# Optimization experiments

Hardware: AMD Instinct MI355X
Metric: run time of the kernel (lower is better)

## Reference

```python
import jax, jax.numpy as jnp
import numpy as np

N = 100000        # nodes
E = 3200000       # edges (avg in-degree ~32)
NG = 64           # graphs in batch
F_IN = 64         # num_node_features
AVG_LOG = float(np.log(33.0))   # avg log-degree baked from deg (avg degree 32)
BN_EPS = 1e-5
STD_EPS = 1e-5

def _glorot(key, fi, fo):
    lim = float(np.sqrt(6.0 / (fi + fo)))
    return jax.random.uniform(key, (fi, fo), jnp.float32, -lim, lim)

def setup_inputs():
    key = jax.random.key(0)
    ks = jax.random.split(key, 16)
    inp = {
        'x': jax.random.normal(ks[0], (N, F_IN), jnp.float32),
        'edge_index': jax.random.randint(ks[1], (2, E), 0, N),
        'batch': jnp.sort(jax.random.randint(ks[2], (N,), 0, NG)),
    }
    dims = [(F_IN, 96), (96, 64), (64, 32), (32, 20)]
    for i, (fi, fo) in enumerate(dims):
        inp[f'w{i}'] = _glorot(ks[3 + i], 13 * fi, fo)  # (4 aggr * 3 scalers + 1 self) * F_in
        inp[f'b{i}'] = jnp.zeros((fo,), jnp.float32)
    for i, c in enumerate([96, 64, 20]):
        inp[f'g{i}'] = jnp.ones((c,), jnp.float32)
        inp[f'be{i}'] = jnp.zeros((c,), jnp.float32)
    inp['w_lin'] = _glorot(ks[10], 20, 11)
    inp['b_lin'] = jnp.zeros((11,), jnp.float32)
    return inp

def _pna_layer(x, src, dst, cnt, degc, W, b):
    m = x[src]                                          # [E, F] gather of neighbor feats
    inv = (1.0 / degc)[:, None]
    mean = jax.ops.segment_sum(m, dst, N) * inv
    mean_sq = jax.ops.segment_sum(m * m, dst, N) * inv
    std = jnp.sqrt(jax.nn.relu(mean_sq - mean * mean) + STD_EPS)
    has = (cnt > 0)[:, None]
    mn = jnp.where(has, jax.ops.segment_min(m, dst, N), 0.0)
    mx = jnp.where(has, jax.ops.segment_max(m, dst, N), 0.0)
    agg = jnp.concatenate([mean, mn, mx, std], axis=-1)  # [N, 4F]
    logd = jnp.log(degc + 1.0)[:, None]
    out = jnp.concatenate([agg, agg * (logd / AVG_LOG), agg * (AVG_LOG / logd)], axis=-1)  # [N, 12F]
    out = jnp.concatenate([x, out], axis=-1)             # [N, 13F] self + scaled aggregations
    return out @ W + b

def _bn(x, g, b):
    mu = x.mean(0)
    var = x.var(0)  # biased var: matches torch BatchNorm training forward
    return (x - mu) * jax.lax.rsqrt(var + BN_EPS) * g + b

def _forward(x, edge_index, batch, w0, b0, w1, b1, w2, b2, w3, b3,
             g0, be0, g1, be1, g2, be2, w_lin, b_lin):
    src, dst = edge_index[0], edge_index[1]
    cnt = jax.ops.segment_sum(jnp.ones((E,), x.dtype), dst, N)  # in-degree
    degc = jnp.maximum(cnt, 1.0)
    h = jax.nn.relu(_bn(_pna_layer(x, src, dst, cnt, degc, w0, b0), g0, be0))
    h = jax.nn.relu(_bn(_pna_layer(h, src, dst, cnt, degc, w1, b1), g1, be1))
    h = jax.nn.relu(_pna_layer(h, src, dst, cnt, degc, w2, b2))
    h = _bn(_pna_layer(h, src, dst, cnt, degc, w3, b3), g2, be2)
    gcnt = jnp.maximum(jax.ops.segment_sum(jnp.ones((N,), h.dtype), batch, NG), 1.0)
    z = jax.ops.segment_sum(h, batch, NG) / gcnt[:, None]       # global mean pool [NG, 20]
    out = jax.nn.softmax(z @ w_lin + b_lin, axis=-1)            # dropout identity (eval)
    return out, z

def reference(x, edge_index, batch, w0, b0, w1, b1, w2, b2, w3, b3,
              g0, be0, g1, be1, g2, be2, w_lin, b_lin):
    return _forward(x, edge_index, batch, w0, b0, w1, b1, w2, b2, w3, b3,
                    g0, be0, g1, be1, g2, be2, w_lin, b_lin)
```

## Files before the change

kernel.cpp:

```cpp
#include <hip/hip_runtime.h>

#define NN 100000
#define NGRAPH 64
#define NPART 8
#define NPB 12500
#define DB 16
#define PW_C 2048
#define AVGLOG 3.4965075614664802f

using f32x2 = __attribute__((ext_vector_type(2))) float;
using f32x4 = __attribute__((ext_vector_type(4))) float;
using f16x2 = __attribute__((ext_vector_type(2))) _Float16;
using f16x8 = __attribute__((ext_vector_type(8))) _Float16;
using f16x4 = __attribute__((ext_vector_type(4))) _Float16;
using i32x4 = __attribute__((ext_vector_type(4))) int;

__global__ __launch_bounds__(256) void k_pcnt(const int* __restrict__ ei,
                                              int* __restrict__ pcnt, int E, int W) {
  const int w = blockIdx.x * 4 + (threadIdx.x >> 6);
  const int lane = threadIdx.x & 63;
  if (w >= W) return;
  int c[NPART];
#pragma unroll
  for (int b = 0; b < NPART; ++b) c[b] = 0;
  const long long base = (long long)w * PW_C;
  for (int r = 0; r < PW_C / 256; ++r) {
    long long e0 = base + r * 256 + lane * 4;
    int bk[4] = {-1, -1, -1, -1};
    if (e0 + 3 < E) {
      i32x4 d = __builtin_nontemporal_load((const i32x4*)(ei + E + e0));
#pragma unroll
      for (int k = 0; k < 4; ++k) bk[k] = d[k] / NPB;
    } else {
#pragma unroll
      for (int k = 0; k < 4; ++k)
        if (e0 + k < E) bk[k] = ei[E + e0 + k] / NPB;
    }
#pragma unroll
    for (int b = 0; b < NPART; ++b) {
      int t = 0;
#pragma unroll
      for (int k = 0; k < 4; ++k) t += __popcll(__ballot(bk[k] == b));
      c[b] += t;
    }
  }
  if (lane == 0) {
#pragma unroll
    for (int b = 0; b < NPART; ++b) pcnt[w * NPART + b] = c[b];
  }
}

__global__ void k_pscan(const int* __restrict__ pcnt, int* __restrict__ pbase,
                        int* __restrict__ bcur, int W) {
  __shared__ int s[256];
  __shared__ int btot[NPART];
  const int t = threadIdx.x;
  const int per = (W + 255) / 256;
  for (int b = 0; b < NPART; ++b) {
    int loc = 0;
    const int w0 = t * per;
    for (int i = 0; i < per; ++i) {
      int w = w0 + i;
      if (w < W) loc += pcnt[w * NPART + b];
    }
    s[t] = loc;
    __syncthreads();
    for (int off = 1; off < 256; off <<= 1) {
      int u = (t >= off) ? s[t - off] : 0;
      __syncthreads();
      s[t] += u;
      __syncthreads();
    }
    int run = s[t] - loc;
    if (t == 255) btot[b] = s[255];
    for (int i = 0; i < per; ++i) {
      int w = w0 + i;
      if (w < W) {
        pbase[w * NPART + b] = run;
        run += pcnt[w * NPART + b];
      }
    }
    __syncthreads();
  }
  if (t < NPART) bcur[t] = btot[t];
}

__global__ __launch_bounds__(256) void k_pbin(const int* __restrict__ ei,
                                              const int* __restrict__ pbase,
                                              unsigned long long* __restrict__ bkt,
                                              int cap, int E, int W) {
  const int w = blockIdx.x * 4 + (threadIdx.x >> 6);
  const int lane = threadIdx.x & 63;
  if (w >= W) return;
  int off[NPART];
#pragma unroll
  for (int b = 0; b < NPART; ++b) off[b] = pbase[w * NPART + b];
  const unsigned long long lmask = (1ull << lane) - 1ull;
  const long long base = (long long)w * PW_C;
  for (int r = 0; r < PW_C / 256; ++r) {
    long long e0 = base + r * 256 + lane * 4;
    int bk[4] = {-1, -1, -1, -1};
    int sv[4], dv[4];
    if (e0 + 3 < E) {
      i32x4 d = __builtin_nontemporal_load((const i32x4*)(ei + E + e0));
      i32x4 s4 = __builtin_nontemporal_load((const i32x4*)(ei + e0));
#pragma unroll
      for (int k = 0; k < 4; ++k) { dv[k] = d[k]; sv[k] = s4[k]; bk[k] = d[k] / NPB; }
    } else {
#pragma unroll
      for (int k = 0; k < 4; ++k)
        if (e0 + k < E) { dv[k] = ei[E + e0 + k]; sv[k] = ei[e0 + k]; bk[k] = dv[k] / NPB; }
    }
#pragma unroll
    for (int k = 0; k < 4; ++k) {
#pragma unroll
      for (int b = 0; b < NPART; ++b) {
        unsigned long long m = __ballot(bk[k] == b);
        if (bk[k] == b) {
          int idx = off[b] + __popcll(m & lmask);
          bkt[(size_t)b * cap + idx] =
              ((unsigned long long)(unsigned)dv[k] << 32) | (unsigned)sv[k];
        }
        off[b] += __popcll(m);
      }
    }
  }
}

__global__ __launch_bounds__(256) void k_dhist(
    const unsigned long long* __restrict__ bkt, const int* __restrict__ bcur,
    int cap, int* __restrict__ dhist) {
  __shared__ int hist[NPB];
  const int p = blockIdx.x & (NPART - 1);
  const int b = blockIdx.x >> 3;
  const int tid = threadIdx.x;
  for (int i = tid; i < NPB; i += 256) hist[i] = 0;
  __syncthreads();
  const int n = bcur[p];
  const int chunk = (n + DB - 1) / DB;
  const int lo = b * chunk, hi = min(n, lo + chunk);
  const unsigned long long* base = bkt + (size_t)p * cap;
  const int plo = p * NPB;
  for (int i = lo + tid; i < hi; i += 256) {
    unsigned long long v = base[i];
    atomicAdd(&hist[(int)(v >> 32) - plo], 1);
  }
  __syncthreads();
  int* dst = dhist + ((size_t)p * DB + b) * NPB;
  for (int i = tid; i < NPB; i += 256) dst[i] = hist[i];
}

__global__ void k_mergesum(int* __restrict__ dhist, int* __restrict__ cnt,
                           int* __restrict__ bsum, int n) {
  __shared__ int s[256];
  int i = blockIdx.x * 256 + threadIdx.x;
  int acc = 0;
  if (i < n) {
    int p = i / NPB, li = i - p * NPB;
    int* hb = dhist + (size_t)p * DB * NPB + li;
#pragma unroll
    for (int b = 0; b < DB; ++b) {
      int t = hb[b * NPB];
      hb[b * NPB] = acc;
      acc += t;
    }
    cnt[i] = acc;
  }
  s[threadIdx.x] = acc;
  __syncthreads();
  for (int off = 128; off > 0; off >>= 1) {
    if (threadIdx.x < off) s[threadIdx.x] += s[threadIdx.x + off];
    __syncthreads();
  }
  if (threadIdx.x == 0) bsum[blockIdx.x] = s[0];
}

__global__ __launch_bounds__(256) void k_binfill(
    const unsigned long long* __restrict__ bkt, const int* __restrict__ bcur,
    int cap, const int* __restrict__ dhist, const int* __restrict__ row_ptr,
    int* __restrict__ colv) {
  __shared__ int rank[NPB];
  const int p = blockIdx.x & (NPART - 1);
  const int b = blockIdx.x >> 3;
  const int tid = threadIdx.x;
  const int plo = p * NPB;
  const int* soff = dhist + ((size_t)p * DB + b) * NPB;
  for (int li = tid; li < NPB; li += 256) rank[li] = row_ptr[plo + li] + soff[li];
  __syncthreads();
  const int n = bcur[p];
  const int chunk = (n + DB - 1) / DB;
  const int lo = b * chunk, hi = min(n, lo + chunk);
  const unsigned long long* base = bkt + (size_t)p * cap;
  for (int i = lo + tid; i < hi; i += 256) {
    unsigned long long v = base[i];
    int d = (int)(v >> 32);
    int s = (int)(v & 0xffffffffu);
    int pos = atomicAdd(&rank[d - plo], 1);
    colv[pos] = s;
  }
}

__global__ void k_scanb(const int* __restrict__ bsum, int* __restrict__ boff, int nb) {
  __shared__ int s[512];
  int t = threadIdx.x;
  int v = (t < nb) ? bsum[t] : 0;
  s[t] = v;
  __syncthreads();
  for (int off = 1; off < 512; off <<= 1) {
    int u = (t >= off) ? s[t - off] : 0;
    __syncthreads();
    s[t] += u;
    __syncthreads();
  }
  if (t < nb) boff[t] = s[t] - v;
}

__global__ void k_scatter(const int* __restrict__ cnt, const int* __restrict__ boff,
                          int* __restrict__ row_ptr, int n, int etot) {
  __shared__ int s[256];
  int i = blockIdx.x * 256 + threadIdx.x;
  int v = (i < n) ? cnt[i] : 0;
  s[threadIdx.x] = v;
  __syncthreads();
  for (int off = 1; off < 256; off <<= 1) {
    int u = (threadIdx.x >= off) ? s[threadIdx.x - off] : 0;
    __syncthreads();
    s[threadIdx.x] += u;
    __syncthreads();
  }
  if (i < n) row_ptr[i] = boff[blockIdx.x] + s[threadIdx.x] - v;
  if (i == 0) row_ptr[n] = etot;
}

__global__ void k_nodesc(const int* __restrict__ cnt, float* __restrict__ invd,
                         float* __restrict__ s1v, float* __restrict__ s2v, int n) {
  int i = blockIdx.x * 256 + threadIdx.x;
  if (i >= n) return;
  float degc = fmaxf((float)cnt[i], 1.f);
  invd[i] = 1.f / degc;
  float ld = logf(degc + 1.f);
  s1v[i] = ld * (1.f / AVGLOG);
  s2v[i] = AVGLOG / ld;
}

__global__ void k_wtprep(const float* __restrict__ W, _Float16* __restrict__ Wt,
                         int K, int FO, int FOP) {
  int i = blockIdx.x * 256 + threadIdx.x;
  if (i >= FOP * K) return;
  int nn = i / K, k = i - nn * K;
  float v = (nn < FO) ? W[k * FO + nn] : 0.f;
  int NT = FOP >> 4;
  int kt = k >> 5, q = (k >> 3) & 3, j = k & 7;
  int nt = nn >> 4, m = nn & 15;
  size_t idx = (((size_t)kt * NT + nt) * 64 + (q * 16 + m)) * 8 + j;
  Wt[idx] = (_Float16)v;
}

__global__ void k_xconv(const float* __restrict__ x, _Float16* __restrict__ x16, int n) {
  int i = blockIdx.x * 256 + threadIdx.x;
  if (i < n) x16[i] = (_Float16)x[i];
}

template <int F, int WPE>
__launch_bounds__(256, WPE)
__global__ void k_agg(const _Float16* __restrict__ hin, const int* __restrict__ row_ptr,
                      const int* __restrict__ colv, const float* __restrict__ invd,
                      _Float16* __restrict__ agg) {
  const int tid = threadIdx.x;
  const int r = tid >> 3, g = tid & 7;
  const int n = blockIdx.x * 32 + r;
  const int e0 = row_ptr[n], e1 = row_ptr[n + 1];
  constexpr int SEG = F / 8;
  constexpr int NP = SEG / 2;
  constexpr int KTA = F / 8;
  f32x2 sm[NP], sq[NP];
  f16x2 mn[NP], mx[NP];
  const _Float16 HPI = __builtin_bit_cast(_Float16, (unsigned short)0x7C00);
  const _Float16 HNI = __builtin_bit_cast(_Float16, (unsigned short)0xFC00);
#pragma unroll
  for (int p = 0; p < NP; ++p) {
    sm[p] = (f32x2){0.f, 0.f};
    sq[p] = (f32x2){0.f, 0.f};
    mn[p] = (f16x2){HPI, HPI};
    mx[p] = (f16x2){HNI, HNI};
  }

  auto loadrow = [&](const _Float16* ra, f16x2* pr) {
    if constexpr (SEG % 8 == 0) {
#pragma unroll
      for (int c = 0; c < SEG / 8; ++c) {
        f16x8 v = ((const f16x8*)ra)[c];
        pr[4 * c + 0] = (f16x2){v[0], v[1]};
        pr[4 * c + 1] = (f16x2){v[2], v[3]};
        pr[4 * c + 2] = (f16x2){v[4], v[5]};
        pr[4 * c + 3] = (f16x2){v[6], v[7]};
      }
    } else {
#pragma unroll
      for (int c = 0; c < SEG / 4; ++c) {
        f16x4 v = ((const f16x4*)ra)[c];
        pr[2 * c + 0] = (f16x2){v[0], v[1]};
        pr[2 * c + 1] = (f16x2){v[2], v[3]};
      }
    }
  };
  auto accum = [&](const f16x2* pr) {
#pragma unroll
    for (int p = 0; p < NP; ++p) {
      f32x2 f = __builtin_convertvector(pr[p], f32x2);
      sm[p] += f;
      sq[p] += f * f;
      mn[p] = __builtin_elementwise_min(mn[p], pr[p]);
      mx[p] = __builtin_elementwise_max(mx[p], pr[p]);
    }
  };

  int e = e0;
  for (; e + 3 < e1; e += 4) {
    int c0 = __builtin_nontemporal_load(&colv[e + 0]);
    int c1 = __builtin_nontemporal_load(&colv[e + 1]);
    int c2 = __builtin_nontemporal_load(&colv[e + 2]);
    int c3 = __builtin_nontemporal_load(&colv[e + 3]);
    f16x2 r0[NP], r1[NP], r2[NP], r3[NP];
    loadrow(hin + (size_t)c0 * F + g * SEG, r0);
    loadrow(hin + (size_t)c1 * F + g * SEG, r1);
    loadrow(hin + (size_t)c2 * F + g * SEG, r2);
    loadrow(hin + (size_t)c3 * F + g * SEG, r3);
    accum(r0);
    accum(r1);
    accum(r2);
    accum(r3);
  }
  for (; e < e1; ++e) {
    int c0 = __builtin_nontemporal_load(&colv[e]);
    f16x2 r0[NP];
    loadrow(hin + (size_t)c0 * F + g * SEG, r0);
    accum(r0);
  }

  float iv = invd[n];
  bool has = (e1 > e0);
  const int m = n & 15;
  const size_t tb = (size_t)(n >> 4) * KTA;
#pragma unroll
  for (int c = 0; c < SEG / 4; ++c) {
    f16x4 vals[4];
#pragma unroll
    for (int l = 0; l < 4; ++l) {
      int j = 4 * c + l;
      int p = j >> 1, k = j & 1;
      float mean = sm[p][k] * iv;
      float var = sq[p][k] * iv - mean * mean;
      float sd = sqrtf(fmaxf(var, 0.f) + 1e-5f);
      vals[0][l] = (_Float16)mean;
      vals[1][l] = has ? mn[p][k] : (_Float16)0.f;
      vals[2][l] = has ? mx[p][k] : (_Float16)0.f;
      vals[3][l] = (_Float16)sd;
    }
    int f0 = g * SEG + 4 * c;
#pragma unroll
    for (int a = 0; a < 4; ++a) {
      int kk0 = a * F + f0;
      int kt = kk0 >> 5, q = (kk0 >> 3) & 3, j0 = kk0 & 7;
      __builtin_nontemporal_store(vals[a],
          (f16x4*)(agg + (tb + kt) * 512 + (q * 16 + m) * 8 + j0));
    }
  }
}

#define MFMA16(a, b, c) __builtin_amdgcn_mfma_f32_16x16x32_f16(a, b, c, 0, 0, 0)

template <int F, int FO, int FOP, bool RELU, bool STATS, typename OT>
__launch_bounds__(256)
__global__ void k_mlp(const _Float16* __restrict__ hin, const _Float16* __restrict__ agg,
                      const float* __restrict__ s1g, const float* __restrict__ s2g,
                      const _Float16* __restrict__ Wt, const float* __restrict__ bias,
                      OT* __restrict__ hout, float* __restrict__ csum,
                      float* __restrict__ csq) {
  constexpr int F32 = F / 32;
  constexpr int KTA = F / 8;
  constexpr int NT = FOP / 16;
  constexpr int PPW = (2 * NT) / 4;
  constexpr int XW = F + 8;
  __shared__ __align__(16) _Float16 s_x[32][XW];
  __shared__ float s_cs[2][FOP];

  const int tid = threadIdx.x;
  const int n0 = blockIdx.x * 32;

  for (int idx = tid; idx < 32 * (F / 8); idx += 256) {
    int r = idx / (F / 8), c = idx % (F / 8);
    *(f16x8*)&s_x[r][8 * c] =
        __builtin_nontemporal_load((const f16x8*)&hin[(size_t)(n0 + r) * F + 8 * c]);
  }
  if (STATS)
    for (int u = tid; u < 2 * FOP; u += 256) (&s_cs[0][0])[u] = 0.f;
  __syncthreads();

  const int w = tid >> 6, ln = tid & 63;
  const int lm = ln & 15, q = ln >> 4;
  const int mt = w & 1;
  const int arow = mt * 16 + lm;
  f32x4 acc0[PPW], acc1[PPW], acc2[PPW];
#pragma unroll
  for (int i = 0; i < PPW; ++i)
#pragma unroll
    for (int t = 0; t < 4; ++t) { acc0[i][t] = 0.f; acc1[i][t] = 0.f; acc2[i][t] = 0.f; }

#pragma unroll
  for (int kt = 0; kt < F32; ++kt) {
    f16x8 a = *(const f16x8*)&s_x[arow][kt * 32 + 8 * q];
#pragma unroll
    for (int i = 0; i < PPW; ++i) {
      int nt = (w >> 1) + 2 * i;
      f16x8 b = *(const f16x8*)&Wt[(((size_t)kt * NT + nt) * 64 + ln) * 8];
      acc0[i] = MFMA16(a, b, acc0[i]);
    }
  }
  const size_t atb = (size_t)(blockIdx.x * 2 + mt) * KTA;
#pragma unroll
  for (int kt = 0; kt < KTA; ++kt) {
    f16x8 a = __builtin_nontemporal_load((const f16x8*)&agg[(atb + kt) * 512 + ln * 8]);
#pragma unroll
    for (int i = 0; i < PPW; ++i) {
      int nt = (w >> 1) + 2 * i;
      f16x8 b0 = *(const f16x8*)&Wt[(((size_t)(F32 + kt) * NT + nt) * 64 + ln) * 8];
      acc0[i] = MFMA16(a, b0, acc0[i]);
      f16x8 b1 = *(const f16x8*)&Wt[(((size_t)(F32 + KTA + kt) * NT + nt) * 64 + ln) * 8];
      acc1[i] = MFMA16(a, b1, acc1[i]);
      f16x8 b2 = *(const f16x8*)&Wt[(((size_t)(F32 + 2 * KTA + kt) * NT + nt) * 64 + ln) * 8];
      acc2[i] = MFMA16(a, b2, acc2[i]);
    }
  }

  float s1r[4], s2r[4];
#pragma unroll
  for (int t = 0; t < 4; ++t) {
    int node = n0 + mt * 16 + q * 4 + t;
    s1r[t] = s1g[node];
    s2r[t] = s2g[node];
  }
#pragma unroll
  for (int i = 0; i < PPW; ++i) {
    int nt = (w >> 1) + 2 * i;
    int ncol = nt * 16 + lm;
    if (FOP == FO || ncol < FO) {
      float bs = bias[ncol];
      float cs = 0.f, cq = 0.f;
#pragma unroll
      for (int t = 0; t < 4; ++t) {
        int node = n0 + mt * 16 + q * 4 + t;
        float v = acc0[i][t] + s1r[t] * acc1[i][t] + s2r[t] * acc2[i][t] + bs;
        if (RELU) v = fmaxf(v, 0.f);
        hout[(size_t)node * FO + ncol] = (OT)v;
        cs += v;
        cq += v * v;
      }
      if (STATS) {
        atomicAdd(&s_cs[0][ncol], cs);
        atomicAdd(&s_cs[1][ncol], cq);
      }
    }
  }
  if (STATS) {
    __syncthreads();
    if (tid < FO) {
      atomicAdd(&csum[tid], s_cs[0][tid]);
      atomicAdd(&csq[tid], s_cs[1][tid]);
    }
  }
}

__global__ void k_bn16(_Float16* __restrict__ h, const float* __restrict__ csum,
                       const float* __restrict__ csq, const float* __restrict__ gg,
                       const float* __restrict__ be, int n, int fo, int relu) {
  int i = blockIdx.x * 256 + threadIdx.x;
  int total = (n * fo) >> 3;
  if (i >= total) return;
  int c0 = (i << 3) % fo;
  float invn = 1.f / (float)n;
  f16x8 v = *(const f16x8*)&h[(size_t)i << 3];
  f16x8 o;
#pragma unroll
  for (int j = 0; j < 8; ++j) {
    int c = c0 + j;
    float mu = csum[c] * invn;
    float var = csq[c] * invn - mu * mu;
    float rs = rsqrtf(var + 1e-5f);
    float x = ((float)v[j] - mu) * rs * gg[c] + be[c];
    if (relu) x = fmaxf(x, 0.f);
    o[j] = (_Float16)x;
  }
  *(f16x8*)&h[(size_t)i << 3] = o;
}

__global__ void k_bnf(float* __restrict__ h, const float* __restrict__ csum,
                      const float* __restrict__ csq, const float* __restrict__ gg,
                      const float* __restrict__ be, int n, int fo, int relu) {
  int i = blockIdx.x * 256 + threadIdx.x;
  if (i >= n * fo) return;
  int c = i % fo;
  float invn = 1.f / (float)n;
  float mu = csum[c] * invn;
  float var = csq[c] * invn - mu * mu;
  float rs = rsqrtf(var + 1e-5f);
  float v = (h[i] - mu) * rs * gg[c] + be[c];
  if (relu) v = fmaxf(v, 0.f);
  h[i] = v;
}

__global__ void k_pool(const float* __restrict__ h, const int* __restrict__ batch,
                       float* __restrict__ zsum, float* __restrict__ gcnt, int n) {
  __shared__ float sv[NGRAPH * 20];
  __shared__ float sc[NGRAPH];
  int tid = threadIdx.x;
  for (int u = tid; u < NGRAPH * 20; u += 256) sv[u] = 0.f;
  if (tid < NGRAPH) sc[tid] = 0.f;
  __syncthreads();
  int i = blockIdx.x * 256 + tid;
  if (i < n) {
    int g = batch[i];
    atomicAdd(&sc[g], 1.f);
    for (int j = 0; j < 20; ++j) atomicAdd(&sv[g * 20 + j], h[(size_t)i * 20 + j]);
  }
  __syncthreads();
  if (tid < NGRAPH && sc[tid] != 0.f) {
    atomicAdd(&gcnt[tid], sc[tid]);
    for (int j = 0; j < 20; ++j) atomicAdd(&zsum[tid * 20 + j], sv[tid * 20 + j]);
  }
}

__global__ void k_head(const float* __restrict__ zsum, const float* __restrict__ gcnt,
                       const float* __restrict__ wl, const float* __restrict__ bl,
                       float* __restrict__ out) {
  int g = threadIdx.x;
  if (g >= NGRAPH) return;
  float z[20];
  float icg = 1.f / fmaxf(gcnt[g], 1.f);
#pragma unroll
  for (int j = 0; j < 20; ++j) {
    z[j] = zsum[g * 20 + j] * icg;
    out[NGRAPH * 11 + g * 20 + j] = z[j];
  }
  float lo[11];
#pragma unroll
  for (int o = 0; o < 11; ++o) {
    float a = bl[o];
    for (int j = 0; j < 20; ++j) a += z[j] * wl[j * 11 + o];
    lo[o] = a;
  }
  float m = lo[0];
  for (int o = 1; o < 11; ++o) m = fmaxf(m, lo[o]);
  float s = 0.f;
  for (int o = 0; o < 11; ++o) { lo[o] = expf(lo[o] - m); s += lo[o]; }
  float is = 1.f / s;
  for (int o = 0; o < 11; ++o) out[g * 11 + o] = lo[o] * is;
}

static inline char* carve(char*& p, size_t bytes) {
  char* r = p;
  p += (bytes + 255) & ~(size_t)255;
  return r;
}

extern "C" void kernel_launch(void* const* d_in, const int* in_sizes, int n_in,
                              void* d_out, int out_size, void* d_ws, size_t ws_size,
                              hipStream_t stream) {
  const float* x = (const float*)d_in[0];
  const int* ei = (const int*)d_in[1];
  const int* batch = (const int*)d_in[2];
  const float* W0 = (const float*)d_in[3];
  const float* b0 = (const float*)d_in[4];
  const float* W1 = (const float*)d_in[5];
  const float* b1 = (const float*)d_in[6];
  const float* W2 = (const float*)d_in[7];
  const float* b2 = (const float*)d_in[8];
  const float* W3 = (const float*)d_in[9];
  const float* b3 = (const float*)d_in[10];
  const float* g0 = (const float*)d_in[11];
  const float* be0 = (const float*)d_in[12];
  const float* g1 = (const float*)d_in[13];
  const float* be1 = (const float*)d_in[14];
  const float* g2 = (const float*)d_in[15];
  const float* be2 = (const float*)d_in[16];
  const float* wl = (const float*)d_in[17];
  const float* bl = (const float*)d_in[18];
  float* out = (float*)d_out;

  const int E = in_sizes[1] / 2;
  const int NB = (NN + 255) / 256;
  const int BCAP = E / NPART + 65536;
  const int W = (E + PW_C - 1) / PW_C;
  const int GB = (W + 3) / 4;

  char* p = (char*)d_ws;
  int* cnt = (int*)carve(p, (size_t)NN * 4);
  int* row_ptr = (int*)carve(p, (size_t)(NN + 1) * 4);
  int* bsum = (int*)carve(p, 2048);
  int* boff = (int*)carve(p, 2048);
  int* bcur = (int*)carve(p, 256);
  int* pcnt = (int*)carve(p, (size_t)W * NPART * 4);
  int* pbase = (int*)carve(p, (size_t)W * NPART * 4);
  int* colv = (int*)carve(p, (size_t)E * 4);
  unsigned long long* bkt = (unsigned long long*)carve(p, (size_t)NPART * BCAP * 8);
  int* dhist = (int*)carve(p, (size_t)NPART * DB * NPB * 4);
  float* invd = (float*)carve(p, (size_t)NN * 4);
  float* s1v = (float*)carve(p, (size_t)NN * 4);
  float* s2v = (float*)carve(p, (size_t)NN * 4);
  _Float16* Wt0 = (_Float16*)carve(p, (size_t)96 * 832 * 2);
  _Float16* Wt1 = (_Float16*)carve(p, (size_t)64 * 1248 * 2);
  _Float16* Wt2 = (_Float16*)carve(p, (size_t)32 * 832 * 2);
  _Float16* Wt3 = (_Float16*)carve(p, (size_t)32 * 416 * 2);
  float* cs = (float*)carve(p, 192 * 4);
  float* csum = cs;
  float* csq = cs + 96;
  float* pacc = (float*)carve(p, (NGRAPH * 20 + NGRAPH) * 4);
  float* zsum = pacc;
  float* gcnt = pacc + NGRAPH * 20;
  _Float16* x16 = (_Float16*)carve(p, (size_t)NN * 64 * 2);
  _Float16* hA16 = (_Float16*)carve(p, (size_t)NN * 96 * 2);
  _Float16* hB16 = (_Float16*)carve(p, (size_t)NN * 96 * 2);
  _Float16* aggb = (_Float16*)carve(p, (size_t)NN * 4 * 96 * 2);
  float* h3 = (float*)x16;

  hipMemsetAsync(pacc, 0, (NGRAPH * 20 + NGRAPH) * 4, stream);
  k_pcnt<<<GB, 256, 0, stream>>>(ei, pcnt, E, W);
  k_pscan<<<1, 256, 0, stream>>>(pcnt, pbase, bcur, W);
  k_pbin<<<GB, 256, 0, stream>>>(ei, pbase, bkt, BCAP, E, W);
  k_dhist<<<NPART * DB, 256, 0, stream>>>(bkt, bcur, BCAP, dhist);
  k_mergesum<<<NB, 256, 0, stream>>>(dhist, cnt, bsum, NN);
  k_scanb<<<1, 512, 0, stream>>>(bsum, boff, NB);
  k_scatter<<<NB, 256, 0, stream>>>(cnt, boff, row_ptr, NN, E);
  k_nodesc<<<NB, 256, 0, stream>>>(cnt, invd, s1v, s2v, NN);
  k_binfill<<<NPART * DB, 256, 0, stream>>>(bkt, bcur, BCAP, dhist, row_ptr, colv);

  k_wtprep<<<(96 * 832 + 255) / 256, 256, 0, stream>>>(W0, Wt0, 832, 96, 96);
  k_wtprep<<<(64 * 1248 + 255) / 256, 256, 0, stream>>>(W1, Wt1, 1248, 64, 64);
  k_wtprep<<<(32 * 832 + 255) / 256, 256, 0, stream>>>(W2, Wt2, 832, 32, 32);
  k_wtprep<<<(32 * 416 + 255) / 256, 256, 0, stream>>>(W3, Wt3, 416, 20, 32);
  k_xconv<<<(NN * 64 + 255) / 256, 256, 0, stream>>>(x, x16, NN * 64);

  const int GP = NN / 32;

  hipMemsetAsync(cs, 0, 192 * 4, stream);
  k_agg<64, 6><<<GP, 256, 0, stream>>>(x16, row_ptr, colv, invd, aggb);
  k_mlp<64, 96, 96, false, true, _Float16><<<GP, 256, 0, stream>>>(x16, aggb, s1v, s2v, Wt0, b0, hA16, csum, csq);
  k_bn16<<<(NN * 96 / 8 + 255) / 256, 256, 0, stream>>>(hA16, csum, csq, g0, be0, NN, 96, 1);

  hipMemsetAsync(cs, 0, 192 * 4, stream);
  k_agg<96, 6><<<GP, 256, 0, stream>>>(hA16, row_ptr, colv, invd, aggb);
  k_mlp<96, 64, 64, false, true, _Float16><<<GP, 256, 0, stream>>>(hA16, aggb, s1v, s2v, Wt1, b1, hB16, csum, csq);
  k_bn16<<<(NN * 64 / 8 + 255) / 256, 256, 0, stream>>>(hB16, csum, csq, g1, be1, NN, 64, 1);

  k_agg<64, 6><<<GP, 256, 0, stream>>>(hB16, row_ptr, colv, invd, aggb);
  k_mlp<64, 32, 32, true, false, _Float16><<<GP, 256, 0, stream>>>(hB16, aggb, s1v, s2v, Wt2, b2, hA16, csum, csq);

  hipMemsetAsync(cs, 0, 192 * 4, stream);
  k_agg<32, 8><<<GP, 256, 0, stream>>>(hA16, row_ptr, colv, invd, aggb);
  k_mlp<32, 20, 32, false, true, float><<<GP, 256, 0, stream>>>(hA16, aggb, s1v, s2v, Wt3, b3, h3, csum, csq);
  k_bnf<<<(NN * 20 + 255) / 256, 256, 0, stream>>>(h3, csum, csq, g2, be2, NN, 20, 0);

  k_pool<<<NB, 256, 0, stream>>>(h3, batch, zsum, gcnt, NN);
  k_head<<<1, 64, 0, stream>>>(zsum, gcnt, wl, bl, out);
}
```

Before: 948.2 us.

## Fuse neighbor aggregation into MLP kernel via shared-memory staging

Merges the separate aggregation and MFMA-based MLP kernels into a single kernel per layer. Aggregated mean/min/max/std are written to shared memory in MFMA tile layout instead of a global buffer, so the large [N,4F] round trip to HBM and one launch per layer go away. The edge loop unroll drops from 4 to 2 and launch bounds change to 2 blocks per CU. This lowers memory-level parallelism for the gather and may reduce occupancy because of the added shared memory and registers.

Result: faster. 866.3 us (-8.6%).

```diff
diff --git a/kernel.cpp b/kernel.cpp
--- a/kernel.cpp
+++ b/kernel.cpp
@@ -261,140 +261,129 @@
   if (i < n) x16[i] = (_Float16)x[i];
 }
 
-template <int F, int WPE>
-__launch_bounds__(256, WPE)
-__global__ void k_agg(const _Float16* __restrict__ hin, const int* __restrict__ row_ptr,
-                      const int* __restrict__ colv, const float* __restrict__ invd,
-                      _Float16* __restrict__ agg) {
-  const int tid = threadIdx.x;
-  const int r = tid >> 3, g = tid & 7;
-  const int n = blockIdx.x * 32 + r;
-  const int e0 = row_ptr[n], e1 = row_ptr[n + 1];
-  constexpr int SEG = F / 8;
-  constexpr int NP = SEG / 2;
-  constexpr int KTA = F / 8;
-  f32x2 sm[NP], sq[NP];
-  f16x2 mn[NP], mx[NP];
-  const _Float16 HPI = __builtin_bit_cast(_Float16, (unsigned short)0x7C00);
-  const _Float16 HNI = __builtin_bit_cast(_Float16, (unsigned short)0xFC00);
-#pragma unroll
-  for (int p = 0; p < NP; ++p) {
-    sm[p] = (f32x2){0.f, 0.f};
-    sq[p] = (f32x2){0.f, 0.f};
-    mn[p] = (f16x2){HPI, HPI};
-    mx[p] = (f16x2){HNI, HNI};
-  }
-
-  auto loadrow = [&](const _Float16* ra, f16x2* pr) {
-    if constexpr (SEG % 8 == 0) {
-#pragma unroll
-      for (int c = 0; c < SEG / 8; ++c) {
-        f16x8 v = ((const f16x8*)ra)[c];
-        pr[4 * c + 0] = (f16x2){v[0], v[1]};
-        pr[4 * c + 1] = (f16x2){v[2], v[3]};
-        pr[4 * c + 2] = (f16x2){v[4], v[5]};
-        pr[4 * c + 3] = (f16x2){v[6], v[7]};
-      }
-    } else {
-#pragma unroll
-      for (int c = 0; c < SEG / 4; ++c) {
-        f16x4 v = ((const f16x4*)ra)[c];
-        pr[2 * c + 0] = (f16x2){v[0], v[1]};
-        pr[2 * c + 1] = (f16x2){v[2], v[3]};
-      }
-    }
-  };
-  auto accum = [&](const f16x2* pr) {
-#pragma unroll
-    for (int p = 0; p < NP; ++p) {
-      f32x2 f = __builtin_convertvector(pr[p], f32x2);
-      sm[p] += f;
-      sq[p] += f * f;
-      mn[p] = __builtin_elementwise_min(mn[p], pr[p]);
-      mx[p] = __builtin_elementwise_max(mx[p], pr[p]);
-    }
-  };
-
-  int e = e0;
-  for (; e + 3 < e1; e += 4) {
-    int c0 = __builtin_nontemporal_load(&colv[e + 0]);
-    int c1 = __builtin_nontemporal_load(&colv[e + 1]);
-    int c2 = __builtin_nontemporal_load(&colv[e + 2]);
-    int c3 = __builtin_nontemporal_load(&colv[e + 3]);
-    f16x2 r0[NP], r1[NP], r2[NP], r3[NP];
-    loadrow(hin + (size_t)c0 * F + g * SEG, r0);
-    loadrow(hin + (size_t)c1 * F + g * SEG, r1);
-    loadrow(hin + (size_t)c2 * F + g * SEG, r2);
-    loadrow(hin + (size_t)c3 * F + g * SEG, r3);
-    accum(r0);
-    accum(r1);
-    accum(r2);
-    accum(r3);
-  }
-  for (; e < e1; ++e) {
-    int c0 = __builtin_nontemporal_load(&colv[e]);
-    f16x2 r0[NP];
-    loadrow(hin + (size_t)c0 * F + g * SEG, r0);
-    accum(r0);
-  }
-
-  float iv = invd[n];
-  bool has = (e1 > e0);
-  const int m = n & 15;
-  const size_t tb = (size_t)(n >> 4) * KTA;
-#pragma unroll
-  for (int c = 0; c < SEG / 4; ++c) {
-    f16x4 vals[4];
-#pragma unroll
-    for (int l = 0; l < 4; ++l) {
-      int j = 4 * c + l;
-      int p = j >> 1, k = j & 1;
-      float mean = sm[p][k] * iv;
-      float var = sq[p][k] * iv - mean * mean;
-      float sd = sqrtf(fmaxf(var, 0.f) + 1e-5f);
-      vals[0][l] = (_Float16)mean;
-      vals[1][l] = has ? mn[p][k] : (_Float16)0.f;
-      vals[2][l] = has ? mx[p][k] : (_Float16)0.f;
-      vals[3][l] = (_Float16)sd;
-    }
-    int f0 = g * SEG + 4 * c;
-#pragma unroll
-    for (int a = 0; a < 4; ++a) {
-      int kk0 = a * F + f0;
-      int kt = kk0 >> 5, q = (kk0 >> 3) & 3, j0 = kk0 & 7;
-      __builtin_nontemporal_store(vals[a],
-          (f16x4*)(agg + (tb + kt) * 512 + (q * 16 + m) * 8 + j0));
-    }
-  }
-}
-
 #define MFMA16(a, b, c) __builtin_amdgcn_mfma_f32_16x16x32_f16(a, b, c, 0, 0, 0)
 
 template <int F, int FO, int FOP, bool RELU, bool STATS, typename OT>
-__launch_bounds__(256)
-__global__ void k_mlp(const _Float16* __restrict__ hin, const _Float16* __restrict__ agg,
-                      const float* __restrict__ s1g, const float* __restrict__ s2g,
-                      const _Float16* __restrict__ Wt, const float* __restrict__ bias,
-                      OT* __restrict__ hout, float* __restrict__ csum,
-                      float* __restrict__ csq) {
+__launch_bounds__(256, 2)
+__global__ void k_fused(const _Float16* __restrict__ hin,
+                        const int* __restrict__ row_ptr, const int* __restrict__ colv,
+                        const float* __restrict__ invd,
+                        const float* __restrict__ s1g, const float* __restrict__ s2g,
+                        const _Float16* __restrict__ Wt, const float* __restrict__ bias,
+                        OT* __restrict__ hout, float* __restrict__ csum,
+                        float* __restrict__ csq) {
   constexpr int F32 = F / 32;
   constexpr int KTA = F / 8;
   constexpr int NT = FOP / 16;
   constexpr int PPW = (2 * NT) / 4;
   constexpr int XW = F + 8;
+  constexpr int SEG = F / 8;
+  constexpr int NP = SEG / 2;
   __shared__ __align__(16) _Float16 s_x[32][XW];
+  __shared__ __align__(16) _Float16 s_a[2 * KTA * 512];
   __shared__ float s_cs[2][FOP];
 
   const int tid = threadIdx.x;
   const int n0 = blockIdx.x * 32;
 
   for (int idx = tid; idx < 32 * (F / 8); idx += 256) {
-    int r = idx / (F / 8), c = idx % (F / 8);
-    *(f16x8*)&s_x[r][8 * c] =
-        __builtin_nontemporal_load((const f16x8*)&hin[(size_t)(n0 + r) * F + 8 * c]);
+    int rr = idx / (F / 8), cc = idx % (F / 8);
+    *(f16x8*)&s_x[rr][8 * cc] = *(const f16x8*)&hin[(size_t)(n0 + rr) * F + 8 * cc];
   }
   if (STATS)
     for (int u = tid; u < 2 * FOP; u += 256) (&s_cs[0][0])[u] = 0.f;
+
+  {
+    const int r = tid >> 3, g = tid & 7;
+    const int n = n0 + r;
+    const int e0 = row_ptr[n], e1 = row_ptr[n + 1];
+    f32x2 sm[NP], sq[NP];
+    f16x2 mn[NP], mx[NP];
+    const _Float16 HPI = __builtin_bit_cast(_Float16, (unsigned short)0x7C00);
+    const _Float16 HNI = __builtin_bit_cast(_Float16, (unsigned short)0xFC00);
+#pragma unroll
+    for (int p = 0; p < NP; ++p) {
+      sm[p] = (f32x2){0.f, 0.f};
+      sq[p] = (f32x2){0.f, 0.f};
+      mn[p] = (f16x2){HPI, HPI};
+      mx[p] = (f16x2){HNI, HNI};
+    }
+
+    auto loadrow = [&](const _Float16* ra, f16x2* pr) {
+      if constexpr (SEG % 8 == 0) {
+#pragma unroll
+        for (int c = 0; c < SEG / 8; ++c) {
+          f16x8 v = ((const f16x8*)ra)[c];
+          pr[4 * c + 0] = (f16x2){v[0], v[1]};
+          pr[4 * c + 1] = (f16x2){v[2], v[3]};
+          pr[4 * c + 2] = (f16x2){v[4], v[5]};
+          pr[4 * c + 3] = (f16x2){v[6], v[7]};
+        }
+      } else {
+#pragma unroll
+        for (int c = 0; c < SEG / 4; ++c) {
+          f16x4 v = ((const f16x4*)ra)[c];
+          pr[2 * c + 0] = (f16x2){v[0], v[1]};
+          pr[2 * c + 1] = (f16x2){v[2], v[3]};
+        }
+      }
+    };
+    auto accum = [&](const f16x2* pr) {
+#pragma unroll
+      for (int p = 0; p < NP; ++p) {
+        f32x2 f = __builtin_convertvector(pr[p], f32x2);
+        sm[p] += f;
+        sq[p] += f * f;
+        mn[p] = __builtin_elementwise_min(mn[p], pr[p]);
+        mx[p] = __builtin_elementwise_max(mx[p], pr[p]);
+      }
+    };
+
+    int e = e0;
+    for (; e + 1 < e1; e += 2) {
+      int c0 = __builtin_nontemporal_load(&colv[e]);
+      int c1 = __builtin_nontemporal_load(&colv[e + 1]);
+      f16x2 r0[NP], r1[NP];
+      loadrow(hin + (size_t)c0 * F + g * SEG, r0);
+      loadrow(hin + (size_t)c1 * F + g * SEG, r1);
+      accum(r0);
+      accum(r1);
+    }
+    if (e < e1) {
+      int c0 = __builtin_nontemporal_load(&colv[e]);
+      f16x2 r0[NP];
+      loadrow(hin + (size_t)c0 * F + g * SEG, r0);
+      accum(r0);
+    }
+
+    float iv = invd[n];
+    bool has = (e1 > e0);
+    const int m = r & 15;
+    const int mt = r >> 4;
+#pragma unroll
+    for (int c = 0; c < SEG / 4; ++c) {
+      f16x4 vals[4];
+#pragma unroll
+      for (int l = 0; l < 4; ++l) {
+        int j = 4 * c + l;
+        int p = j >> 1, k = j & 1;
+        float mean = sm[p][k] * iv;
+        float var = sq[p][k] * iv - mean * mean;
+        float sd = sqrtf(fmaxf(var, 0.f) + 1e-5f);
+        vals[0][l] = (_Float16)mean;
+        vals[1][l] = has ? mn[p][k] : (_Float16)0.f;
+        vals[2][l] = has ? mx[p][k] : (_Float16)0.f;
+        vals[3][l] = (_Float16)sd;
+      }
+      int f0 = g * SEG + 4 * c;
+#pragma unroll
+      for (int a = 0; a < 4; ++a) {
+        int kk0 = a * F + f0;
+        int kt = kk0 >> 5, q = (kk0 >> 3) & 3, j0 = kk0 & 7;
+        *(f16x4*)&s_a[((size_t)(mt * KTA + kt)) * 512 + (q * 16 + m) * 8 + j0] = vals[a];
+      }
+    }
+  }
   __syncthreads();
 
   const int w = tid >> 6, ln = tid & 63;
@@ -417,10 +406,9 @@
       acc0[i] = MFMA16(a, b, acc0[i]);
     }
   }
-  const size_t atb = (size_t)(blockIdx.x * 2 + mt) * KTA;
 #pragma unroll
   for (int kt = 0; kt < KTA; ++kt) {
-    f16x8 a = __builtin_nontemporal_load((const f16x8*)&agg[(atb + kt) * 512 + ln * 8]);
+    f16x8 a = *(const f16x8*)&s_a[((size_t)(mt * KTA + kt)) * 512 + ln * 8];
 #pragma unroll
     for (int i = 0; i < PPW; ++i) {
       int nt = (w >> 1) + 2 * i;
@@ -620,7 +608,6 @@
   _Float16* x16 = (_Float16*)carve(p, (size_t)NN * 64 * 2);
   _Float16* hA16 = (_Float16*)carve(p, (size_t)NN * 96 * 2);
   _Float16* hB16 = (_Float16*)carve(p, (size_t)NN * 96 * 2);
-  _Float16* aggb = (_Float16*)carve(p, (size_t)NN * 4 * 96 * 2);
   float* h3 = (float*)x16;
 
   hipMemsetAsync(pacc, 0, (NGRAPH * 20 + NGRAPH) * 4, stream);
@@ -643,21 +630,21 @@
   const int GP = NN / 32;
 
   hipMemsetAsync(cs, 0, 192 * 4, stream);
-  k_agg<64, 6><<<GP, 256, 0, stream>>>(x16, row_ptr, colv, invd, aggb);
-  k_mlp<64, 96, 96, false, true, _Float16><<<GP, 256, 0, stream>>>(x16, aggb, s1v, s2v, Wt0, b0, hA16, csum, csq);
+  k_fused<64, 96, 96, false, true, _Float16><<<GP, 256, 0, stream>>>(
+      x16, row_ptr, colv, invd, s1v, s2v, Wt0, b0, hA16, csum, csq);
   k_bn16<<<(NN * 96 / 8 + 255) / 256, 256, 0, stream>>>(hA16, csum, csq, g0, be0, NN, 96, 1);
 
   hipMemsetAsync(cs, 0, 192 * 4, stream);
-  k_agg<96, 6><<<GP, 256, 0, stream>>>(hA16, row_ptr, colv, invd, aggb);
-  k_mlp<96, 64, 64, false, true, _Float16><<<GP, 256, 0, stream>>>(hA16, aggb, s1v, s2v, Wt1, b1, hB16, csum, csq);
+  k_fused<96, 64, 64, false, true, _Float16><<<GP, 256, 0, stream>>>(
+      hA16, row_ptr, colv, invd, s1v, s2v, Wt1, b1, hB16, csum, csq);
   k_bn16<<<(NN * 64 / 8 + 255) / 256, 256, 0, stream>>>(hB16, csum, csq, g1, be1, NN, 64, 1);
 
-  k_agg<64, 6><<<GP, 256, 0, stream>>>(hB16, row_ptr, colv, invd, aggb);
-  k_mlp<64, 32, 32, true, false, _Float16><<<GP, 256, 0, stream>>>(hB16, aggb, s1v, s2v, Wt2, b2, hA16, csum, csq);
+  k_fused<64, 32, 32, true, false, _Float16><<<GP, 256, 0, stream>>>(
+      hB16, row_ptr, colv, invd, s1v, s2v, Wt2, b2, hA16, csum, csq);
 
   hipMemsetAsync(cs, 0, 192 * 4, stream);
-  k_agg<32, 8><<<GP, 256, 0, stream>>>(hA16, row_ptr, colv, invd, aggb);
-  k_mlp<32, 20, 32, false, true, float><<<GP, 256, 0, stream>>>(hA16, aggb, s1v, s2v, Wt3, b3, h3, csum, csq);
+  k_fused<32, 20, 32, false, true, float><<<GP, 256, 0, stream>>>(
+      hA16, row_ptr, colv, invd, s1v, s2v, Wt3, b3, h3, csum, csq);
   k_bnf<<<(NN * 20 + 255) / 256, 256, 0, stream>>>(h3, csum, csq, g2, be2, NN, 20, 0);
 
   k_pool<<<NB, 256, 0, stream>>>(h3, batch, zsum, gcnt, NN);
```
